# Performance work log

Measured on AMD Instinct MI355X. Metric: run time of the kernel, lower is better.

Reference implementation:

```python
import jax, jax.numpy as jnp
import numpy as np

DIM = 1152
NUM_HEADS = 16
HEAD_DIM = DIM // NUM_HEADS
EPS = 1e-6
B, N, M = 4, 4096, 512


def setup_inputs() -> dict:
    key = jax.random.key(0)
    ks = jax.random.split(key, 12)
    s = 0.02
    return {
        "x": jax.random.normal(ks[0], (B, N, DIM), dtype=jnp.float32),
        "cond": jax.random.normal(ks[1], (B, M, DIM), dtype=jnp.float32),
        "kv_seqlen": jax.random.randint(ks[2], (B,), 1, M + 1, dtype=jnp.int32),
        "q_w": jax.random.normal(ks[3], (DIM, DIM), dtype=jnp.float32) * s,
        "q_b": jnp.zeros((DIM,), jnp.float32),
        "kv_w": jax.random.normal(ks[4], (DIM, 2 * DIM), dtype=jnp.float32) * s,
        "kv_b": jnp.zeros((2 * DIM,), jnp.float32),
        "proj_w": jax.random.normal(ks[5], (DIM, DIM), dtype=jnp.float32) * s,
        "proj_b": jnp.zeros((DIM,), jnp.float32),
        "qn_w": jnp.ones((HEAD_DIM,), jnp.float32),
        "kn_w": jnp.ones((HEAD_DIM,), jnp.float32),
    }


def _rmsnorm_fp32(t, w):
    # RMSNorm computed in fp32 over head_dim, then cast back
    t32 = t.astype(jnp.float32)
    inv = jax.lax.rsqrt(jnp.mean(t32 * t32, axis=-1, keepdims=True) + EPS)
    return ((t32 * inv) * w.astype(jnp.float32)).astype(t.dtype)


def reference(x, cond, kv_seqlen, q_w, q_b, kv_w, kv_b, proj_w, proj_b, qn_w, kn_w):
    b, n, c = x.shape
    out_dtype = x.dtype
    q = (x @ q_w + q_b).reshape(b, n, NUM_HEADS, HEAD_DIM)           # [B,N,H,D]
    kv = (cond @ kv_w + kv_b).reshape(b, -1, 2, NUM_HEADS, HEAD_DIM)
    k, v = kv[:, :, 0], kv[:, :, 1]                                   # [B,M,H,D]
    q = _rmsnorm_fp32(q, qn_w)
    k = _rmsnorm_fp32(k, kn_w)
    # original casts to bf16 for the attention kernel when out_dtype is fp32
    q16, k16, v16 = q.astype(jnp.bfloat16), k.astype(jnp.bfloat16), v.astype(jnp.bfloat16)
    scale = 1.0 / np.sqrt(HEAD_DIM)
    scores = jnp.einsum("bnhd,bmhd->bhnm", q16, k16,
                        preferred_element_type=jnp.float32) * scale   # [B,H,N,M] fp32
    m = cond.shape[1]
    valid = (jnp.arange(m)[None, :] < kv_seqlen[:, None])             # [B,M] ragged kv mask
    scores = jnp.where(valid[:, None, None, :], scores, -jnp.inf)
    probs = jax.nn.softmax(scores, axis=-1).astype(jnp.bfloat16)
    out = jnp.einsum("bhnm,bmhd->bnhd", probs, v16).reshape(b, n, c)
    out = out.astype(out_dtype)
    return out @ proj_w + proj_b
```

## Files before the change

### kernel.cpp

```cpp
#include <hip/hip_runtime.h>
#include <math.h>

typedef unsigned short ushort_t;
typedef __attribute__((ext_vector_type(4))) float floatx4;
typedef __attribute__((ext_vector_type(8))) short bf16x8;

#define DIMC 1152
#define NHEADS 16
#define HDIM 72

__device__ __forceinline__ ushort_t f2bf(float f) {
  unsigned u = __float_as_uint(f);
  u += 0x7FFFu + ((u >> 16) & 1u);
  return (ushort_t)(u >> 16);
}
__device__ __forceinline__ float bf2f(ushort_t s) {
  return __uint_as_float(((unsigned)s) << 16);
}

__device__ __forceinline__ void gload_lds16(const ushort_t* g, ushort_t* l) {
  __builtin_amdgcn_global_load_lds(
      (const __attribute__((address_space(1))) unsigned int*)(const void*)g,
      (__attribute__((address_space(3))) unsigned int*)(void*)l, 16, 0, 0);
}

__device__ __forceinline__ bf16x8 load_bf16x8(const ushort_t* p) {
  union { bf16x8 v; uint4 u; } t;
  t.u = *(const uint4*)p;
  return t.v;
}

__global__ void cvt_bf16_kernel(const float* __restrict__ src,
                                ushort_t* __restrict__ dst, int n8) {
  int i = blockIdx.x * 256 + threadIdx.x;
  if (i >= n8) return;
  float4 f0 = ((const float4*)src)[2 * (size_t)i];
  float4 f1 = ((const float4*)src)[2 * (size_t)i + 1];
  union { ushort_t s[8]; uint4 u; } t;
  t.s[0] = f2bf(f0.x); t.s[1] = f2bf(f0.y); t.s[2] = f2bf(f0.z); t.s[3] = f2bf(f0.w);
  t.s[4] = f2bf(f1.x); t.s[5] = f2bf(f1.y); t.s[6] = f2bf(f1.z); t.s[7] = f2bf(f1.w);
  ((uint4*)dst)[i] = t.u;
}

__global__ void transpose_w_kernel(const float* __restrict__ W,
                                   ushort_t* __restrict__ Wt, int K, int N) {
  __shared__ ushort_t tile[64 * 80];
  int k0 = blockIdx.x * 64, n0 = blockIdx.y * 64;
  int tid = threadIdx.x;
  int kl = tid >> 4, n4 = tid & 15;
  for (int rr = 0; rr < 4; rr++) {
    int k = kl + rr * 16;
    float4 f = *(const float4*)(W + (size_t)(k0 + k) * N + n0 + n4 * 4);
    tile[(n4 * 4 + 0) * 80 + k] = f2bf(f.x);
    tile[(n4 * 4 + 1) * 80 + k] = f2bf(f.y);
    tile[(n4 * 4 + 2) * 80 + k] = f2bf(f.z);
    tile[(n4 * 4 + 3) * 80 + k] = f2bf(f.w);
  }
  __syncthreads();
  int nl = tid >> 2, kq = tid & 3;
  uint4 v0 = *(const uint4*)(tile + nl * 80 + kq * 16);
  uint4 v1 = *(const uint4*)(tile + nl * 80 + kq * 16 + 8);
  *(uint4*)(Wt + (size_t)(n0 + nl) * K + k0 + kq * 16) = v0;
  *(uint4*)(Wt + (size_t)(n0 + nl) * K + k0 + kq * 16 + 8) = v1;
}

template <bool OUT_F32>
__global__ __launch_bounds__(256, 2) void gemm128_kernel(
    const ushort_t* __restrict__ A0, const ushort_t* __restrict__ Bt0,
    const float* __restrict__ bias0, void* __restrict__ C0,
    int NTn0, int Ncols0,
    const ushort_t* __restrict__ A1, const ushort_t* __restrict__ Bt1,
    const float* __restrict__ bias1, void* __restrict__ C1,
    int NTn1, int Ncols1,
    int nblk0, int Kdim) {
  __shared__ ushort_t S[32768];

  int lin = blockIdx.x;
  int cpx = gridDim.x >> 3;
  int wg = (lin & 7) * cpx + (lin >> 3);

  const ushort_t* Aseg; const ushort_t* Bseg;
  const float* bias; void* Cptr; int NTn, Ncols;
  if (wg < nblk0) {
    Aseg = A0; Bseg = Bt0; bias = bias0; Cptr = C0; NTn = NTn0; Ncols = Ncols0;
  } else {
    wg -= nblk0;
    Aseg = A1; Bseg = Bt1; bias = bias1; Cptr = C1; NTn = NTn1; Ncols = Ncols1;
  }
  int mt = wg / NTn, nt = wg % NTn;
  int m0 = mt * 128, n0 = nt * 128;

  int tid = threadIdx.x;
  int wid = tid >> 6, lane = tid & 63, quad = lane >> 4, l16 = lane & 15;
  int wr = wid >> 1, wc = wid & 1;
  const int qoff = (quad * 8) ^ ((l16 & 8) << 1);

  const int srow = tid >> 2;
  const int scol = ((tid & 3) * 8) ^ ((tid & 32) ? 16 : 0);
  const ushort_t* Abase = Aseg + (size_t)m0 * Kdim;
  const ushort_t* Bbase = Bseg + (size_t)n0 * Kdim;

  auto stageA = [&](int t, int ks) {
    const ushort_t* src = Abase + (size_t)srow * Kdim + t * 64 + ks * 32 + scol;
    ushort_t* dst = S + (t & 1) * 16384 + ks * 4096 + (tid >> 6) * 512;
    gload_lds16(src, dst);
    gload_lds16(src + (size_t)64 * Kdim, dst + 2048);
  };
  auto stageB = [&](int t, int ks) {
    const ushort_t* src = Bbase + (size_t)srow * Kdim + t * 64 + ks * 32 + scol;
    ushort_t* dst = S + (t & 1) * 16384 + 8192 + ks * 4096 + (tid >> 6) * 512;
    gload_lds16(src, dst);
    gload_lds16(src + (size_t)64 * Kdim, dst + 2048);
  };

  floatx4 zero = {0.f, 0.f, 0.f, 0.f};
  floatx4 acc[4][4];
#pragma unroll
  for (int i = 0; i < 4; i++)
#pragma unroll
    for (int j = 0; j < 4; j++) acc[i][j] = zero;

  int NT = Kdim >> 6;

  stageA(0, 0); stageB(0, 0);
  stageA(0, 1); stageB(0, 1);
  asm volatile("s_waitcnt vmcnt(4)" ::: "memory");
  __builtin_amdgcn_s_barrier();

  for (int t = 0; t < NT; ++t) {
    const int abase = (t & 1) * 16384;
    const int arow = (wr * 64 + l16) * 32 + qoff;
    const int brow = (wc * 64 + l16) * 32 + qoff;

#pragma unroll
    for (int ks = 0; ks < 2; ++ks) {
      const int ab = abase + ks * 4096;
      const int bb = abase + 8192 + ks * 4096;
      bf16x8 af[4], bfr[4];
#pragma unroll
      for (int mf = 0; mf < 4; mf++)
        af[mf] = *(const bf16x8*)(S + ab + arow + mf * 512);
#pragma unroll
      for (int c = 0; c < 4; c++)
        bfr[c] = *(const bf16x8*)(S + bb + brow + c * 512);
      if (t + 1 < NT) { stageA(t + 1, ks); stageB(t + 1, ks); }
      __builtin_amdgcn_s_barrier();
      asm volatile("s_waitcnt lgkmcnt(0)" ::: "memory");
      __builtin_amdgcn_sched_barrier(0);
      __builtin_amdgcn_s_setprio(1);
#pragma unroll
      for (int c = 0; c < 4; c++)
#pragma unroll
        for (int mf = 0; mf < 4; mf++)
          acc[mf][c] = __builtin_amdgcn_mfma_f32_16x16x32_bf16(af[mf], bfr[c], acc[mf][c], 0, 0, 0);
      __builtin_amdgcn_s_setprio(0);
      if (t + 1 < NT)
        asm volatile("s_waitcnt vmcnt(4)" ::: "memory");
      else
        asm volatile("s_waitcnt vmcnt(0)" ::: "memory");
      __builtin_amdgcn_s_barrier();
    }
  }

  float bv[4];
#pragma unroll
  for (int c = 0; c < 4; c++) bv[c] = bias[n0 + wc * 64 + c * 16 + l16];
#pragma unroll
  for (int mf = 0; mf < 4; mf++)
#pragma unroll
    for (int c = 0; c < 4; c++)
#pragma unroll
      for (int r = 0; r < 4; r++) {
        int row = m0 + wr * 64 + mf * 16 + quad * 4 + r;
        int col = n0 + wc * 64 + c * 16 + l16;
        float v = acc[mf][c][r] + bv[c];
        if constexpr (OUT_F32)
          ((float*)Cptr)[(size_t)row * Ncols + col] = v;
        else
          ((ushort_t*)Cptr)[(size_t)row * Ncols + col] = f2bf(v);
      }
}

__global__ void rmsnorm_heads_kernel(ushort_t* __restrict__ p,
                                     const float* __restrict__ w,
                                     int rowstride) {
  int gw = blockIdx.x * 4 + (threadIdx.x >> 6);
  int lane = threadIdx.x & 63;
  int row = gw >> 4, h = gw & 15;
  ushort_t* base = p + (size_t)row * rowstride + h * HDIM;
  float v0 = bf2f(base[lane]);
  float v1 = (lane < 8) ? bf2f(base[64 + lane]) : 0.f;
  float ss = v0 * v0 + v1 * v1;
  for (int off = 1; off < 64; off <<= 1) ss += __shfl_xor(ss, off);
  float inv = rsqrtf(ss / 72.0f + 1e-6f);
  base[lane] = f2bf(v0 * inv * w[lane]);
  if (lane < 8) base[64 + lane] = f2bf(v1 * inv * w[64 + lane]);
}

__global__ void vtrans_kernel(const ushort_t* __restrict__ kv16,
                              ushort_t* __restrict__ vT) {
  __shared__ ushort_t tile[64 * 84];
  int b = blockIdx.z, h = blockIdx.y, m0 = blockIdx.x * 64;
  int tid = threadIdx.x;
  int row = tid >> 2, sl = tid & 3;
  const ushort_t* src =
      kv16 + (size_t)(b * 512 + m0 + row) * 2304 + DIMC + h * HDIM;
#pragma unroll
  for (int k = 0; k < 5; k++) {
    int s = sl + 4 * k;
    if (s < 18) {
      uint2 v = *(const uint2*)(src + s * 4);
      *(uint2*)(tile + row * 84 + s * 4) = v;
    }
  }
  __syncthreads();
  size_t dbase = (size_t)((b * 16 + h) * 80) * 512 + m0;
#pragma unroll
  for (int it = 0; it < 5; it++) {
    int idx = it * 256 + tid;
    int d = idx >> 4, mseg = idx & 15;
    union { ushort_t s[4]; uint2 u; } pk;
    if (d < HDIM) {
      pk.s[0] = tile[(mseg * 4 + 0) * 84 + d];
      pk.s[1] = tile[(mseg * 4 + 1) * 84 + d];
      pk.s[2] = tile[(mseg * 4 + 2) * 84 + d];
      pk.s[3] = tile[(mseg * 4 + 3) * 84 + d];
    } else {
      ushort_t f = (d == HDIM) ? (ushort_t)0x3F80 : (ushort_t)0;
      pk.s[0] = pk.s[1] = pk.s[2] = pk.s[3] = f;
    }
    *(uint2*)(vT + dbase + (size_t)d * 512 + mseg * 4) = pk.u;
  }
}

__global__ __launch_bounds__(256, 4) void attn_kernel(
    const ushort_t* __restrict__ q16, const ushort_t* __restrict__ kv16,
    const ushort_t* __restrict__ vT, const int* __restrict__ seqlens,
    const float* __restrict__ qn_w, ushort_t* __restrict__ att) {
  __shared__ ushort_t KV[22 * 512];
  __shared__ ushort_t Ps[4][32 * 64];
  int b = blockIdx.z, h = blockIdx.y, n0 = blockIdx.x * 128;
  int tid = threadIdx.x, wid = tid >> 6, lane = tid & 63;
  int quad = lane >> 4, l16 = lane & 15;
  int seqlen = seqlens[b];
  const float qscale = 0.11785113019775793f * 1.44269504088896f;

  ushort_t* Pw = &Ps[wid][0];

  bf16x8 qf[2][3];
  float ssq[2] = {0.f, 0.f};
  for (int rb = 0; rb < 2; rb++)
    for (int ks = 0; ks < 3; ks++) {
      if (ks == 2 && quad > 0) {
        qf[rb][ks] = (bf16x8){0, 0, 0, 0, 0, 0, 0, 0};
      } else {
        size_t off = ((size_t)(b * 4096 + n0 + wid * 32 + rb * 16 + l16)) * DIMC +
                     h * HDIM + ks * 32 + quad * 8;
        qf[rb][ks] = load_bf16x8(q16 + off);
        union { bf16x8 v; ushort_t s[8]; } e;
        e.v = qf[rb][ks];
        for (int j = 0; j < 8; j++) {
          float x = bf2f(e.s[j]);
          ssq[rb] += x * x;
        }
      }
    }
  for (int rb = 0; rb < 2; rb++) {
    ssq[rb] += __shfl_xor(ssq[rb], 16);
    ssq[rb] += __shfl_xor(ssq[rb], 32);
  }
  for (int rb = 0; rb < 2; rb++) {
    float inv = rsqrtf(ssq[rb] / 72.0f + 1e-6f) * qscale;
    for (int ks = 0; ks < 3; ks++) {
      if (ks == 2 && quad > 0) continue;
      float4 w0 = *(const float4*)(qn_w + ks * 32 + quad * 8);
      float4 w1 = *(const float4*)(qn_w + ks * 32 + quad * 8 + 4);
      union { bf16x8 v; ushort_t s[8]; } e;
      e.v = qf[rb][ks];
      e.s[0] = f2bf(bf2f(e.s[0]) * inv * w0.x);
      e.s[1] = f2bf(bf2f(e.s[1]) * inv * w0.y);
      e.s[2] = f2bf(bf2f(e.s[2]) * inv * w0.z);
      e.s[3] = f2bf(bf2f(e.s[3]) * inv * w0.w);
      e.s[4] = f2bf(bf2f(e.s[4]) * inv * w1.x);
      e.s[5] = f2bf(bf2f(e.s[5]) * inv * w1.y);
      e.s[6] = f2bf(bf2f(e.s[6]) * inv * w1.z);
      e.s[7] = f2bf(bf2f(e.s[7]) * inv * w1.w);
      qf[rb][ks] = e.v;
    }
  }

  floatx4 zero = {0.f, 0.f, 0.f, 0.f};
  floatx4 of[2][5];
  for (int rb = 0; rb < 2; rb++)
    for (int nf = 0; nf < 5; nf++) of[rb][nf] = zero;

  const size_t kvrow = (size_t)b * 512;
  const size_t vbase = (size_t)((b * 16 + h) * 80) * 512;

  int ntiles = (seqlen + 63) >> 6;
  for (int mt = 0; mt < ntiles; mt++) {
    int m0 = mt * 64;

    __syncthreads();
    for (int id = wid; id < 22; id += 4) {
      const ushort_t* src;
      if (id < 12) {
        int c = (id * 11) >> 5;
        int ks = id - c * 3;
        src = kv16 + (size_t)(kvrow + m0 + c * 16 + l16) * 2304 + h * HDIM +
              ks * 32 + quad * 8;
      } else {
        int v = id - 12;
        int nf = v >> 1, ks = v & 1;
        src = vT + (vbase + (size_t)(nf * 16 + l16) * 512) + m0 + ks * 32 + quad * 8;
      }
      gload_lds16(src, KV + id * 512);
    }
    __syncthreads();

    floatx4 sf[2][4];
    for (int rb = 0; rb < 2; rb++)
      for (int c = 0; c < 4; c++) sf[rb][c] = zero;
    for (int c = 0; c < 4; c++)
      for (int ks = 0; ks < 3; ks++) {
        bf16x8 kf = *(const bf16x8*)(KV + (c * 3 + ks) * 512 + lane * 8);
        for (int rb = 0; rb < 2; rb++)
          sf[rb][c] = __builtin_amdgcn_mfma_f32_16x16x32_bf16(qf[rb][ks], kf, sf[rb][c], 0, 0, 0);
      }

    for (int rb = 0; rb < 2; rb++)
      for (int c = 0; c < 4; c++) {
        bool valid = (m0 + c * 16 + l16) < seqlen;
        int col = (c * 16 + l16) ^ (quad * 16);
        int rowb = rb * 16 + quad * 4;
        for (int r = 0; r < 4; r++) {
          float pp = valid ? __builtin_amdgcn_exp2f(sf[rb][c][r]) : 0.f;
          Pw[(rowb + r) * 64 + col] = f2bf(pp);
        }
      }

    for (int ks = 0; ks < 2; ks++) {
      bf16x8 pf[2];
      int g = ((ks * 2 + (quad >> 1)) * 16 + (quad & 1) * 8) ^ (((l16 >> 2) & 3) * 16);
      for (int rb = 0; rb < 2; rb++)
        pf[rb] = *(const bf16x8*)(Pw + (rb * 16 + l16) * 64 + g);
      for (int nf = 0; nf < 5; nf++) {
        bf16x8 vf = *(const bf16x8*)(KV + (12 + nf * 2 + ks) * 512 + lane * 8);
        for (int rb = 0; rb < 2; rb++)
          of[rb][nf] = __builtin_amdgcn_mfma_f32_16x16x32_bf16(pf[rb], vf, of[rb][nf], 0, 0, 0);
      }
    }
  }

  for (int rb = 0; rb < 2; rb++) {
    float invl[4];
    for (int r = 0; r < 4; r++) {
      float lsum = __shfl(of[rb][4][r], (lane & 48) | 8);
      invl[r] = 1.0f / lsum;
    }
    for (int nf = 0; nf < 5; nf++) {
      int d = nf * 16 + l16;
      if (d < HDIM) {
        for (int r = 0; r < 4; r++) {
          size_t o = ((size_t)(b * 4096 + n0 + wid * 32 + rb * 16 + quad * 4 + r)) * DIMC +
                     h * HDIM + d;
          att[o] = f2bf(of[rb][nf][r] * invl[r]);
        }
      }
    }
  }
}

extern "C" void kernel_launch(void* const* d_in, const int* in_sizes, int n_in,
                              void* d_out, int out_size, void* d_ws, size_t ws_size,
                              hipStream_t stream) {
  const float* x      = (const float*)d_in[0];
  const float* cond   = (const float*)d_in[1];
  const int*   seqlen = (const int*)d_in[2];
  const float* q_w    = (const float*)d_in[3];
  const float* q_b    = (const float*)d_in[4];
  const float* kv_w   = (const float*)d_in[5];
  const float* kv_b   = (const float*)d_in[6];
  const float* proj_w = (const float*)d_in[7];
  const float* proj_b = (const float*)d_in[8];
  const float* qn_w   = (const float*)d_in[9];
  const float* kn_w   = (const float*)d_in[10];
  float* out = (float*)d_out;

  char* ws = (char*)d_ws;
  size_t o = 0;
  ushort_t* qwT    = (ushort_t*)(ws + o); o += (size_t)1152 * 1152 * 2;
  ushort_t* kvwT   = (ushort_t*)(ws + o); o += (size_t)2304 * 1152 * 2;
  ushort_t* pwT    = (ushort_t*)(ws + o); o += (size_t)1152 * 1152 * 2;
  ushort_t* q16    = (ushort_t*)(ws + o); o += (size_t)16384 * 1152 * 2;
  ushort_t* kv16   = (ushort_t*)(ws + o); o += (size_t)2048 * 2304 * 2;
  ushort_t* vT     = (ushort_t*)(ws + o); o += (size_t)64 * 80 * 512 * 2;
  ushort_t* att    = (ushort_t*)(ws + o); o += (size_t)16384 * 1152 * 2;
  ushort_t* x16    = (ushort_t*)(ws + o); o += (size_t)16384 * 1152 * 2;
  ushort_t* cond16 = (ushort_t*)(ws + o); o += (size_t)2048 * 1152 * 2;

  dim3 blk(256);

  cvt_bf16_kernel<<<dim3((16384 * 1152 / 8 + 255) / 256), blk, 0, stream>>>(
      x, x16, 16384 * 1152 / 8);
  cvt_bf16_kernel<<<dim3((2048 * 1152 / 8 + 255) / 256), blk, 0, stream>>>(
      cond, cond16, 2048 * 1152 / 8);

  transpose_w_kernel<<<dim3(1152 / 64, 1152 / 64), blk, 0, stream>>>(q_w, qwT, 1152, 1152);
  transpose_w_kernel<<<dim3(1152 / 64, 2304 / 64), blk, 0, stream>>>(kv_w, kvwT, 1152, 2304);
  transpose_w_kernel<<<dim3(1152 / 64, 1152 / 64), blk, 0, stream>>>(proj_w, pwT, 1152, 1152);

  gemm128_kernel<false><<<dim3(1152 + 288), blk, 0, stream>>>(
      x16, qwT, q_b, q16, 9, 1152,
      cond16, kvwT, kv_b, kv16, 18, 2304,
      1152, 1152);

  rmsnorm_heads_kernel<<<dim3(2048 * 16 / 4), blk, 0, stream>>>(kv16, kn_w, 2304);

  vtrans_kernel<<<dim3(8, 16, 4), blk, 0, stream>>>(kv16, vT);

  attn_kernel<<<dim3(32, 16, 4), blk, 0, stream>>>(q16, kv16, vT, seqlen, qn_w, att);

  gemm128_kernel<true><<<dim3(1152), blk, 0, stream>>>(
      att, pwT, proj_b, out, 9, 1152,
      att, pwT, proj_b, out, 9, 1152,
      1152, 1152);
}
```

Before: 380.9 us.

## Merge prep and K-norm/V-transpose launches; transpose score MFMA for packed P stores

Combines the two fp32→bf16 conversions and three weight transposes into one launch, and the K RMSNorm and V transpose into another, to cut kernel launch and tail overhead. In attention, the score MFMA operands are swapped so each lane holds four consecutive keys for one query. Probabilities are then packed with v_cvt_pk_bf16_f32 and written as 8-byte stores into an XOR-swizzled LDS buffer, replacing scalar 2-byte stores. The per-element seqlen mask now runs only on tiles that cross the sequence end. The cost is extra branching on block index in the merged kernels and inline asm that ties the code to this target.

```diff
diff --git a/kernel.cpp b/kernel.cpp
--- a/kernel.cpp
+++ b/kernel.cpp
@@ -30,23 +30,35 @@
   return t.v;
 }
 
-__global__ void cvt_bf16_kernel(const float* __restrict__ src,
-                                ushort_t* __restrict__ dst, int n8) {
-  int i = blockIdx.x * 256 + threadIdx.x;
-  if (i >= n8) return;
-  float4 f0 = ((const float4*)src)[2 * (size_t)i];
-  float4 f1 = ((const float4*)src)[2 * (size_t)i + 1];
-  union { ushort_t s[8]; uint4 u; } t;
-  t.s[0] = f2bf(f0.x); t.s[1] = f2bf(f0.y); t.s[2] = f2bf(f0.z); t.s[3] = f2bf(f0.w);
-  t.s[4] = f2bf(f1.x); t.s[5] = f2bf(f1.y); t.s[6] = f2bf(f1.z); t.s[7] = f2bf(f1.w);
-  ((uint4*)dst)[i] = t.u;
-}
-
-__global__ void transpose_w_kernel(const float* __restrict__ W,
-                                   ushort_t* __restrict__ Wt, int K, int N) {
+__global__ void prep_kernel(const float* __restrict__ x, ushort_t* __restrict__ x16,
+                            const float* __restrict__ cond, ushort_t* __restrict__ cond16,
+                            const float* __restrict__ q_w, ushort_t* __restrict__ qwT,
+                            const float* __restrict__ kv_w, ushort_t* __restrict__ kvwT,
+                            const float* __restrict__ proj_w, ushort_t* __restrict__ pwT) {
   __shared__ ushort_t tile[64 * 80];
-  int k0 = blockIdx.x * 64, n0 = blockIdx.y * 64;
+  int blk = blockIdx.x;
   int tid = threadIdx.x;
+
+  if (blk < 10368) {
+    const float* src; ushort_t* dst; int i;
+    if (blk < 9216) { src = x; dst = x16; i = blk * 256 + tid; }
+    else            { src = cond; dst = cond16; i = (blk - 9216) * 256 + tid; }
+    float4 f0 = ((const float4*)src)[2 * (size_t)i];
+    float4 f1 = ((const float4*)src)[2 * (size_t)i + 1];
+    union { ushort_t s[8]; uint4 u; } t;
+    t.s[0] = f2bf(f0.x); t.s[1] = f2bf(f0.y); t.s[2] = f2bf(f0.z); t.s[3] = f2bf(f0.w);
+    t.s[4] = f2bf(f1.x); t.s[5] = f2bf(f1.y); t.s[6] = f2bf(f1.z); t.s[7] = f2bf(f1.w);
+    ((uint4*)dst)[i] = t.u;
+    return;
+  }
+
+  const float* W; ushort_t* Wt; int N, idx;
+  if (blk < 10692)      { W = q_w;    Wt = qwT;  N = 1152; idx = blk - 10368; }
+  else if (blk < 11340) { W = kv_w;   Wt = kvwT; N = 2304; idx = blk - 10692; }
+  else                  { W = proj_w; Wt = pwT;  N = 1152; idx = blk - 11340; }
+  const int K = 1152;
+  int k0 = (idx % 18) * 64, n0 = (idx / 18) * 64;
+
   int kl = tid >> 4, n4 = tid & 15;
   for (int rr = 0; rr < 4; rr++) {
     int k = kl + rr * 16;
@@ -181,27 +193,30 @@
       }
 }
 
-__global__ void rmsnorm_heads_kernel(ushort_t* __restrict__ p,
-                                     const float* __restrict__ w,
-                                     int rowstride) {
-  int gw = blockIdx.x * 4 + (threadIdx.x >> 6);
-  int lane = threadIdx.x & 63;
-  int row = gw >> 4, h = gw & 15;
-  ushort_t* base = p + (size_t)row * rowstride + h * HDIM;
-  float v0 = bf2f(base[lane]);
-  float v1 = (lane < 8) ? bf2f(base[64 + lane]) : 0.f;
-  float ss = v0 * v0 + v1 * v1;
-  for (int off = 1; off < 64; off <<= 1) ss += __shfl_xor(ss, off);
-  float inv = rsqrtf(ss / 72.0f + 1e-6f);
-  base[lane] = f2bf(v0 * inv * w[lane]);
-  if (lane < 8) base[64 + lane] = f2bf(v1 * inv * w[64 + lane]);
-}
-
-__global__ void vtrans_kernel(const ushort_t* __restrict__ kv16,
-                              ushort_t* __restrict__ vT) {
+__global__ void rmsvt_kernel(ushort_t* __restrict__ kv16,
+                             const float* __restrict__ kn_w,
+                             ushort_t* __restrict__ vT) {
   __shared__ ushort_t tile[64 * 84];
-  int b = blockIdx.z, h = blockIdx.y, m0 = blockIdx.x * 64;
+  int blk = blockIdx.x;
   int tid = threadIdx.x;
+
+  if (blk < 8192) {
+    int gw = blk * 4 + (tid >> 6);
+    int lane = tid & 63;
+    int row = gw >> 4, h = gw & 15;
+    ushort_t* base = kv16 + (size_t)row * 2304 + h * HDIM;
+    float v0 = bf2f(base[lane]);
+    float v1 = (lane < 8) ? bf2f(base[64 + lane]) : 0.f;
+    float ss = v0 * v0 + v1 * v1;
+    for (int off = 1; off < 64; off <<= 1) ss += __shfl_xor(ss, off);
+    float inv = rsqrtf(ss / 72.0f + 1e-6f);
+    base[lane] = f2bf(v0 * inv * kn_w[lane]);
+    if (lane < 8) base[64 + lane] = f2bf(v1 * inv * kn_w[64 + lane]);
+    return;
+  }
+
+  int idx = blk - 8192;
+  int m0 = (idx & 7) * 64, h = (idx >> 3) & 15, b = idx >> 7;
   int row = tid >> 2, sl = tid & 3;
   const ushort_t* src =
       kv16 + (size_t)(b * 512 + m0 + row) * 2304 + DIMC + h * HDIM;
@@ -217,8 +232,8 @@
   size_t dbase = (size_t)((b * 16 + h) * 80) * 512 + m0;
 #pragma unroll
   for (int it = 0; it < 5; it++) {
-    int idx = it * 256 + tid;
-    int d = idx >> 4, mseg = idx & 15;
+    int i2 = it * 256 + tid;
+    int d = i2 >> 4, mseg = i2 & 15;
     union { ushort_t s[4]; uint2 u; } pk;
     if (d < HDIM) {
       pk.s[0] = tile[(mseg * 4 + 0) * 84 + d];
@@ -238,14 +253,15 @@
     const ushort_t* __restrict__ vT, const int* __restrict__ seqlens,
     const float* __restrict__ qn_w, ushort_t* __restrict__ att) {
   __shared__ ushort_t KV[22 * 512];
-  __shared__ ushort_t Ps[4][32 * 64];
+  __shared__ __align__(16) unsigned Ps[4][32 * 32];
   int b = blockIdx.z, h = blockIdx.y, n0 = blockIdx.x * 128;
   int tid = threadIdx.x, wid = tid >> 6, lane = tid & 63;
   int quad = lane >> 4, l16 = lane & 15;
   int seqlen = seqlens[b];
   const float qscale = 0.11785113019775793f * 1.44269504088896f;
 
-  ushort_t* Pw = &Ps[wid][0];
+  unsigned* Pw = &Ps[wid][0];
+  const int xorm = (l16 & 7) << 2;
 
   bf16x8 qf[2][3];
   float ssq[2] = {0.f, 0.f};
@@ -260,8 +276,8 @@
         union { bf16x8 v; ushort_t s[8]; } e;
         e.v = qf[rb][ks];
         for (int j = 0; j < 8; j++) {
-          float x = bf2f(e.s[j]);
-          ssq[rb] += x * x;
+          float xv = bf2f(e.s[j]);
+          ssq[rb] += xv * xv;
         }
       }
     }
@@ -325,25 +341,38 @@
       for (int ks = 0; ks < 3; ks++) {
         bf16x8 kf = *(const bf16x8*)(KV + (c * 3 + ks) * 512 + lane * 8);
         for (int rb = 0; rb < 2; rb++)
-          sf[rb][c] = __builtin_amdgcn_mfma_f32_16x16x32_bf16(qf[rb][ks], kf, sf[rb][c], 0, 0, 0);
-      }
-
-    for (int rb = 0; rb < 2; rb++)
+          sf[rb][c] = __builtin_amdgcn_mfma_f32_16x16x32_bf16(kf, qf[rb][ks], sf[rb][c], 0, 0, 0);
+      }
+
+    bool partial = (m0 + 64) > seqlen;
+    for (int rb = 0; rb < 2; rb++) {
+      unsigned* prow = Pw + (rb * 16 + l16) * 32;
       for (int c = 0; c < 4; c++) {
-        bool valid = (m0 + c * 16 + l16) < seqlen;
-        int col = (c * 16 + l16) ^ (quad * 16);
-        int rowb = rb * 16 + quad * 4;
-        for (int r = 0; r < 4; r++) {
-          float pp = valid ? __builtin_amdgcn_exp2f(sf[rb][c][r]) : 0.f;
-          Pw[(rowb + r) * 64 + col] = f2bf(pp);
+        float p0 = __builtin_amdgcn_exp2f(sf[rb][c][0]);
+        float p1 = __builtin_amdgcn_exp2f(sf[rb][c][1]);
+        float p2 = __builtin_amdgcn_exp2f(sf[rb][c][2]);
+        float p3 = __builtin_amdgcn_exp2f(sf[rb][c][3]);
+        if (partial) {
+          int kabs = m0 + c * 16 + quad * 4;
+          p0 = (kabs < seqlen) ? p0 : 0.f;
+          p1 = (kabs + 1 < seqlen) ? p1 : 0.f;
+          p2 = (kabs + 2 < seqlen) ? p2 : 0.f;
+          p3 = (kabs + 3 < seqlen) ? p3 : 0.f;
         }
-      }
+        unsigned w0, w1;
+        asm("v_cvt_pk_bf16_f32 %0, %1, %2" : "=v"(w0) : "v"(p0), "v"(p1));
+        asm("v_cvt_pk_bf16_f32 %0, %1, %2" : "=v"(w1) : "v"(p2), "v"(p3));
+        uint2 pw2; pw2.x = w0; pw2.y = w1;
+        *(uint2*)(prow + ((8 * c + 2 * quad) ^ xorm)) = pw2;
+      }
+    }
 
     for (int ks = 0; ks < 2; ks++) {
       bf16x8 pf[2];
-      int g = ((ks * 2 + (quad >> 1)) * 16 + (quad & 1) * 8) ^ (((l16 >> 2) & 3) * 16);
-      for (int rb = 0; rb < 2; rb++)
-        pf[rb] = *(const bf16x8*)(Pw + (rb * 16 + l16) * 64 + g);
+      for (int rb = 0; rb < 2; rb++) {
+        const unsigned* prow = Pw + (rb * 16 + l16) * 32;
+        pf[rb] = *(const bf16x8*)(prow + ((ks * 16 + quad * 4) ^ xorm));
+      }
       for (int nf = 0; nf < 5; nf++) {
         bf16x8 vf = *(const bf16x8*)(KV + (12 + nf * 2 + ks) * 512 + lane * 8);
         for (int rb = 0; rb < 2; rb++)
@@ -401,23 +430,15 @@
 
   dim3 blk(256);
 
-  cvt_bf16_kernel<<<dim3((16384 * 1152 / 8 + 255) / 256), blk, 0, stream>>>(
-      x, x16, 16384 * 1152 / 8);
-  cvt_bf16_kernel<<<dim3((2048 * 1152 / 8 + 255) / 256), blk, 0, stream>>>(
-      cond, cond16, 2048 * 1152 / 8);
-
-  transpose_w_kernel<<<dim3(1152 / 64, 1152 / 64), blk, 0, stream>>>(q_w, qwT, 1152, 1152);
-  transpose_w_kernel<<<dim3(1152 / 64, 2304 / 64), blk, 0, stream>>>(kv_w, kvwT, 1152, 2304);
-  transpose_w_kernel<<<dim3(1152 / 64, 1152 / 64), blk, 0, stream>>>(proj_w, pwT, 1152, 1152);
+  prep_kernel<<<dim3(11664), blk, 0, stream>>>(
+      x, x16, cond, cond16, q_w, qwT, kv_w, kvwT, proj_w, pwT);
 
   gemm128_kernel<false><<<dim3(1152 + 288), blk, 0, stream>>>(
       x16, qwT, q_b, q16, 9, 1152,
       cond16, kvwT, kv_b, kv16, 18, 2304,
       1152, 1152);
 
-  rmsnorm_heads_kernel<<<dim3(2048 * 16 / 4), blk, 0, stream>>>(kv16, kn_w, 2304);
-
-  vtrans_kernel<<<dim3(8, 16, 4), blk, 0, stream>>>(kv16, vT);
+  rmsvt_kernel<<<dim3(8192 + 512), blk, 0, stream>>>(kv16, kn_w, vT);
 
   attn_kernel<<<dim3(32, 16, 4), blk, 0, stream>>>(q16, kv16, vT, seqlen, qn_w, att);
 
```

Measured after the change: 360.2 us. -5.4%, faster.
